# Optimization experiments

Hardware: AMD Instinct MI355X
Metric: run time of the kernel (lower is better)

Reference implementation:

```python
import jax, jax.numpy as jnp
import numpy as np
import math

B, M, N, K = 4, 8192, 8192, 16
FD = 64       # in_fdim == out_fdim (residual add)
HID = 128     # args.hidden_dim
G = 8         # args.ngroups


def index_points(points, idx):
    # points: (B, C, N), idx: (B, M, K) -> (B, C, M, K)
    return jax.vmap(lambda p, i: p[:, i])(points, idx)


def conv1d(x, w, b):  # 1x1 Conv1d: x (B,Ci,M), w (Co,Ci)
    return jnp.einsum('oi,bim->bom', w, x) + b[None, :, None]


def conv2d(x, w, b):  # 1x1 Conv2d: x (B,Ci,M,K), w (Co,Ci)
    return jnp.einsum('oi,bimk->bomk', w, x) + b[None, :, None, None]


def group_norm(x, w, b, eps=1e-5):
    # torch GroupNorm over (C//G, M, K) per group per sample
    Bb, C, Mm, Kk = x.shape
    xr = x.reshape(Bb, G, C // G, Mm, Kk)
    mu = xr.mean(axis=(2, 3, 4), keepdims=True)
    var = xr.var(axis=(2, 3, 4), keepdims=True)
    xr = (xr - mu) * jax.lax.rsqrt(var + eps)
    return xr.reshape(Bb, C, Mm, Kk) * w[None, :, None, None] + b[None, :, None, None]


def setup_inputs() -> dict:
    key = jax.random.key(0)
    ks = jax.random.split(key, 24)
    s = 0.05
    inp = {
        'q_xyzs': jax.random.normal(ks[0], (B, 3, M), jnp.float32),
        'k_xyzs': jax.random.normal(ks[1], (B, 3, N), jnp.float32),
        'q_feats': jax.random.normal(ks[2], (B, FD, M), jnp.float32),
        'k_feats': jax.random.normal(ks[3], (B, FD, N), jnp.float32),
        'v_feats': jax.random.normal(ks[4], (B, FD, N), jnp.float32),
        'knn_idx': jax.random.randint(ks[5], (B, M, K), 0, N),
        'mask': jnp.ones((B, M, K), dtype=bool),
        'wq_w': jax.random.normal(ks[6], (HID, FD)) * s, 'wq_b': jnp.zeros((HID,)),
        'wk_w': jax.random.normal(ks[7], (HID, FD)) * s, 'wk_b': jnp.zeros((HID,)),
        'wv_w': jax.random.normal(ks[8], (HID, FD)) * s, 'wv_b': jnp.zeros((HID,)),
        'd1_w': jax.random.normal(ks[9], (HID, 3)) * s, 'd1_b': jnp.zeros((HID,)),
        'dgn_w': jnp.ones((HID,)), 'dgn_b': jnp.zeros((HID,)),
        'd2_w': jax.random.normal(ks[10], (HID, HID)) * s, 'd2_b': jnp.zeros((HID,)),
        'g1_w': jax.random.normal(ks[11], (HID, HID)) * s, 'g1_b': jnp.zeros((HID,)),
        'ggn_w': jnp.ones((HID,)), 'ggn_b': jnp.zeros((HID,)),
        'g2_w': jax.random.normal(ks[12], (HID, HID)) * s, 'g2_b': jnp.zeros((HID,)),
        'post_w': jax.random.normal(ks[13], (FD, HID)) * s, 'post_b': jnp.zeros((FD,)),
    }
    return inp


def reference(q_xyzs, k_xyzs, q_feats, k_feats, v_feats, knn_idx, mask,
              wq_w, wq_b, wk_w, wk_b, wv_w, wv_b,
              d1_w, d1_b, dgn_w, dgn_b, d2_w, d2_b,
              g1_w, g1_b, ggn_w, ggn_b, g2_w, g2_b,
              post_w, post_b):
    knn_xyzs = index_points(k_xyzs, knn_idx)                 # (B,3,M,K)
    pre = q_feats
    query = conv1d(q_feats, wq_w, wq_b)                      # (B,HID,M)
    key = index_points(conv1d(k_feats, wk_w, wk_b), knn_idx) # (B,HID,M,K)
    value = index_points(conv1d(v_feats, wv_w, wv_b), knn_idx)

    rel = q_xyzs[:, :, :, None] - knn_xyzs                   # (B,3,M,K)
    pos_enc = conv2d(jax.nn.relu(group_norm(conv2d(rel, d1_w, d1_b), dgn_w, dgn_b)), d2_w, d2_b)

    attn_in = query[:, :, :, None] - key + pos_enc
    attn = conv2d(jax.nn.relu(group_norm(conv2d(attn_in, g1_w, g1_b), ggn_w, ggn_b)), g2_w, g2_b)
    attn = attn / math.sqrt(HID)
    attn = jnp.where(mask[:, None], attn, -jnp.finfo(attn.dtype).max)
    attn = jax.nn.softmax(attn, axis=-1)                     # over neighbor axis K

    res = jnp.einsum('bcmk,bcmk->bcm', attn, value + pos_enc)
    return conv1d(res, post_w, post_b) + pre
```

## Files before the change

kernel.cpp:

```cpp
#include <hip/hip_runtime.h>
#include <hip/hip_bf16.h>

typedef __attribute__((ext_vector_type(8))) short short8;
typedef __attribute__((ext_vector_type(4))) float f32x4;
typedef unsigned short ushort_t;

#define B_    4
#define M_    8192
#define N_    8192
#define KNN   16
#define FD    64
#define HID   128
#define CNT   (M_*KNN)
#define SCALE 0.08838834764831845f

#define QT_OFF       0ULL
#define KT_OFF       4194304ULL
#define VT_OFF       6291456ULL
#define WD2_OFF      8388608ULL
#define WG1_OFF      8396800ULL
#define WG2_OFF      8404992ULL
#define WQT_OFF      8413184ULL
#define WKT_OFF      8421376ULL
#define WVT_OFF      8429568ULL
#define POSTT_OFF    8437760ULL
#define G2BS_OFF     8445952ULL
#define HAFF_OFF     8446080ULL
#define RELSTATS_OFF 8448128ULL
#define YSUM_OFF     8448192ULL
#define YSQ_OFF      8448704ULL
#define GGNA_OFF     8449216ULL
#define GGNB_OFF     8449728ULL

__device__ __forceinline__ ushort_t f2bf(float x) {
    union { float f; unsigned u; } v; v.f = x;
    unsigned r = (v.u + 0x7FFFu + ((v.u >> 16) & 1u)) >> 16;
    return (ushort_t)r;
}
__device__ __forceinline__ float bf2f(ushort_t b) {
    union { unsigned u; float f; } v; v.u = ((unsigned)b) << 16;
    return v.f;
}

__global__ __launch_bounds__(256) void k_wswz(
    const float* __restrict__ d2, const float* __restrict__ g1, const float* __restrict__ g2,
    const float* __restrict__ post, const float* __restrict__ g2b,
    const float* __restrict__ wq, const float* __restrict__ wk, const float* __restrict__ wv,
    float* __restrict__ ws)
{
    int tid = blockIdx.x * 256 + threadIdx.x;
    if (tid < 16384) {
        int j = tid & 7, lane = (tid >> 3) & 63, s = (tid >> 9) & 3, ct = tid >> 11;
        int row = ct*16 + (lane & 15);
        int colk = s*32 + (lane >> 4)*8 + j;
        int si = row*HID + colk;
        ((ushort_t*)(ws + WD2_OFF))[tid] = f2bf(d2[si]);
        ((ushort_t*)(ws + WG1_OFF))[tid] = f2bf(g1[si]);
        ((ushort_t*)(ws + WG2_OFF))[tid] = f2bf(g2[si] * SCALE);
    }
    if (tid < 8192) {
        int f = tid >> 7, j = tid & 127;
        ws[POSTT_OFF + j*64 + f] = post[tid];
        int i = tid >> 7, c = tid & 127;
        ws[WQT_OFF + tid] = wq[c*FD + i];
        ws[WKT_OFF + tid] = wk[c*FD + i];
        ws[WVT_OFF + tid] = wv[c*FD + i];
    }
    if (tid < 128) ws[G2BS_OFF + tid] = g2b[tid] * SCALE;
}

__global__ __launch_bounds__(256) void k_transform(
    const float* __restrict__ qf, const float* __restrict__ kf, const float* __restrict__ vf,
    const float* __restrict__ wq_b, const float* __restrict__ wk_b, const float* __restrict__ wv_b,
    float* __restrict__ ws)
{
    __shared__ __align__(16) float sF[64*36];
    int tid = threadIdx.x;
    int t = blockIdx.y;
    int gm0 = blockIdx.x * 32;
    int b = gm0 >> 13, m0 = gm0 & (M_-1);
    const float* in = (t==0) ? qf : (t==1) ? kf : vf;
    const float* wT = ws + ((t==0) ? WQT_OFF : (t==1) ? WKT_OFF : WVT_OFF);
    const float* bi = (t==0) ? wq_b : (t==1) ? wk_b : wv_b;
    {
        int i = tid >> 2, sg = tid & 3;
        const float* src = in + ((size_t)b*FD + i)*M_ + m0 + sg*8;
        f32x4 a = *(const f32x4*)src;
        f32x4 c = *(const f32x4*)(src + 4);
        *(f32x4*)&sF[i*36 + sg*8]     = a;
        *(f32x4*)&sF[i*36 + sg*8 + 4] = c;
    }
    __syncthreads();
    int c = tid & 127, h = tid >> 7;
    float acc[16];
    float bc = bi[c];
    #pragma unroll
    for (int p = 0; p < 16; p++) acc[p] = bc;
    #pragma unroll 4
    for (int i = 0; i < 64; i++) {
        float w = wT[i*128 + c];
        #pragma unroll
        for (int pq = 0; pq < 4; pq++) {
            f32x4 fv = *(const f32x4*)&sF[i*36 + h*16 + pq*4];
            acc[pq*4+0] += w*fv[0]; acc[pq*4+1] += w*fv[1];
            acc[pq*4+2] += w*fv[2]; acc[pq*4+3] += w*fv[3];
        }
    }
    if (t == 0) {
        #pragma unroll
        for (int p = 0; p < 16; p++)
            ws[QT_OFF + (size_t)(gm0 + h*16 + p)*HID + c] = acc[p];
    } else {
        ushort_t* o = (ushort_t*)(ws + ((t==1) ? KT_OFF : VT_OFF));
        #pragma unroll
        for (int p = 0; p < 16; p++)
            o[(size_t)(gm0 + h*16 + p)*HID + c] = f2bf(acc[p]);
    }
}

__global__ __launch_bounds__(256) void k_relstats(
    const float* __restrict__ qx, const float* __restrict__ kx,
    const int* __restrict__ knn, float* __restrict__ ws)
{
    int tid = threadIdx.x;
    int b = blockIdx.y;
    int m = blockIdx.x * 256 + tid;
    const float* qb = qx + (size_t)b*3*M_;
    const float* kb = kx + (size_t)b*3*N_;
    const int* kn = knn + ((size_t)b*M_ + m)*KNN;
    float a[9] = {0,0,0,0,0,0,0,0,0};
    float q0 = qb[m], q1 = qb[M_+m], q2 = qb[2*M_+m];
    #pragma unroll
    for (int k = 0; k < KNN; k++) {
        int id = kn[k];
        float r0 = q0 - kb[id], r1 = q1 - kb[N_+id], r2 = q2 - kb[2*N_+id];
        a[0]+=r0; a[1]+=r1; a[2]+=r2;
        a[3]+=r0*r0; a[4]+=r0*r1; a[5]+=r0*r2;
        a[6]+=r1*r1; a[7]+=r1*r2; a[8]+=r2*r2;
    }
    __shared__ float red[4];
    float* rs = ws + RELSTATS_OFF + b*16;
    for (int q = 0; q < 9; q++) {
        float v = a[q];
        #pragma unroll
        for (int o = 32; o > 0; o >>= 1) v += __shfl_down(v, o, 64);
        if ((tid & 63) == 0) red[tid >> 6] = v;
        __syncthreads();
        if (tid == 0) atomicAdd(&rs[q], red[0]+red[1]+red[2]+red[3]);
        __syncthreads();
    }
}

__global__ __launch_bounds__(512) void k_dgn(
    const float* __restrict__ d1w, const float* __restrict__ d1b,
    const float* __restrict__ gw, const float* __restrict__ gb,
    float* __restrict__ ws)
{
    __shared__ float sm[512], sq[512], smu[32], srs[32];
    int t = threadIdx.x, b = t >> 7, c = t & 127;
    const float* rs = ws + RELSTATS_OFF + b*16;
    float inv = 1.0f / (float)CNT;
    float x0 = rs[0]*inv, x1 = rs[1]*inv, x2 = rs[2]*inv;
    float S00 = rs[3]*inv, S01 = rs[4]*inv, S02 = rs[5]*inv;
    float S11 = rs[6]*inv, S12 = rs[7]*inv, S22 = rs[8]*inv;
    float w0 = d1w[c*3], w1 = d1w[c*3+1], w2 = d1w[c*3+2], bc = d1b[c];
    float mc = w0*x0 + w1*x1 + w2*x2 + bc;
    float qc = w0*w0*S00 + w1*w1*S11 + w2*w2*S22
             + 2.f*(w0*w1*S01 + w0*w2*S02 + w1*w2*S12)
             + 2.f*bc*(mc - bc) + bc*bc;
    sm[t] = mc; sq[t] = qc;
    __syncthreads();
    if (t < 32) {
        int bb = t >> 3, g = t & 7;
        float mu = 0, ey = 0;
        for (int j = 0; j < 16; j++) { mu += sm[bb*128 + g*16 + j]; ey += sq[bb*128 + g*16 + j]; }
        mu *= (1.f/16.f); ey *= (1.f/16.f);
        smu[t] = mu; srs[t] = rsqrtf(ey - mu*mu + 1e-5f);
    }
    __syncthreads();
    int g = c >> 4;
    float al = gw[c] * srs[b*8 + g];
    float be = gb[c] - smu[b*8 + g] * al;
    f32x4 h; h[0] = al*w0; h[1] = al*w1; h[2] = al*w2; h[3] = al*bc + be;
    *(f32x4*)(ws + HAFF_OFF + ((size_t)b*128 + c)*4) = h;
}

__global__ __launch_bounds__(512) void k_ggn(
    const float* __restrict__ gw, const float* __restrict__ gb, float* __restrict__ ws)
{
    __shared__ float smu[32], srs[32];
    int t = threadIdx.x, b = t >> 7, c = t & 127;
    if (t < 32) {
        int bb = t >> 3, g = t & 7;
        float s1 = 0, s2 = 0;
        for (int j = 0; j < 16; j++) {
            s1 += ws[YSUM_OFF + bb*128 + g*16 + j];
            s2 += ws[YSQ_OFF  + bb*128 + g*16 + j];
        }
        float invn = 1.f / (16.f * (float)CNT);
        float mu = s1*invn, ey = s2*invn;
        smu[t] = mu; srs[t] = rsqrtf(ey - mu*mu + 1e-5f);
    }
    __syncthreads();
    int g = c >> 4;
    float al = gw[c] * srs[b*8 + g];
    float be = gb[c] - smu[b*8 + g] * al;
    ws[GGNA_OFF + b*128 + c] = al;
    ws[GGNB_OFF + b*128 + c] = be;
}

template<bool STATS>
__global__ __launch_bounds__(256, 3) void k_pipe(
    const float* __restrict__ qx, const float* __restrict__ kx, const int* __restrict__ knn,
    const float* __restrict__ qf,
    const float* __restrict__ d2b, const float* __restrict__ g1b, const float* __restrict__ postb,
    float* __restrict__ ws, float* __restrict__ out)
{
    __shared__ __align__(16) ushort_t tP[4][16*136];
    __shared__ __align__(16) ushort_t tAY[4][16*136];
    __shared__ __align__(16) f32x4 sHaff[128];
    __shared__ __align__(16) float sQR[4][128];
    __shared__ __align__(16) float sGa[128], sGb[128];
    __shared__ __align__(16) float sRel[4][16][4];
    __shared__ int sIdx[64];
    __shared__ __align__(16) float sOut[4][64];

    int tid = threadIdx.x, wid = tid >> 6, lane = tid & 63;
    int n = lane & 15, q = lane >> 4;
    int gm0 = blockIdx.x * 4;
    int b = gm0 >> 13;
    int m0 = gm0 & (M_-1);
    int ct0 = wid * 2;

    const ushort_t* ktb = (const ushort_t*)(ws + KT_OFF);
    const ushort_t* vtb = (const ushort_t*)(ws + VT_OFF);

    if (tid < 64) {
        int id = knn[(size_t)gm0*KNN + tid];
        sIdx[tid] = id;
        int p = tid >> 4, nn = tid & 15;
        int m = m0 + p;
        sRel[p][nn][0] = qx[(size_t)b*3*M_ + m]        - kx[(size_t)b*3*N_ + id];
        sRel[p][nn][1] = qx[(size_t)b*3*M_ + M_ + m]   - kx[(size_t)b*3*N_ + N_ + id];
        sRel[p][nn][2] = qx[(size_t)b*3*M_ + 2*M_ + m] - kx[(size_t)b*3*N_ + 2*N_ + id];
    }
    if (tid < 128) {
        sHaff[tid] = *(const f32x4*)(ws + HAFF_OFF + ((size_t)b*128 + tid)*4);
        if (STATS) { sGa[tid] = 0.f; sGb[tid] = 0.f; }
        else { sGa[tid] = ws[GGNA_OFF + b*128 + tid]; sGb[tid] = ws[GGNB_OFF + b*128 + tid]; }
        *(f32x4*)(&sQR[0][0] + tid*4) = *(const f32x4*)(ws + QT_OFF + (size_t)gm0*HID + tid*4);
    }
    __syncthreads();

    {
        const short8* wA = (const short8*)(ws + WD2_OFF);
        short8 wf[2][4];
        #pragma unroll
        for (int cc = 0; cc < 2; cc++)
            #pragma unroll
            for (int s = 0; s < 4; s++)
                wf[cc][s] = wA[((ct0+cc)*4 + s)*64 + lane];
        #pragma unroll
        for (int p = 0; p < 4; p++) {
            f32x4 rv = *(const f32x4*)sRel[p][n];
            short8 bh[4];
            #pragma unroll
            for (int s = 0; s < 4; s++)
                #pragma unroll
                for (int j = 0; j < 8; j++) {
                    f32x4 hf = sHaff[s*32 + q*8 + j];
                    float h = fmaf(hf[0], rv[0], fmaf(hf[1], rv[1], fmaf(hf[2], rv[2], hf[3])));
                    bh[s][j] = (short)f2bf(h > 0.f ? h : 0.f);
                }
            #pragma unroll
            for (int cc = 0; cc < 2; cc++) {
                f32x4 acc = {0.f,0.f,0.f,0.f};
                #pragma unroll
                for (int s = 0; s < 4; s++)
                    acc = __builtin_amdgcn_mfma_f32_16x16x32_bf16(wf[cc][s], bh[s], acc, 0,0,0);
                int row0 = (ct0+cc)*16 + q*4;
                f32x4 bi = *(const f32x4*)(d2b + row0);
                uint2 pv;
                pv.x = (unsigned)f2bf(acc[0]+bi[0]) | ((unsigned)f2bf(acc[1]+bi[1]) << 16);
                pv.y = (unsigned)f2bf(acc[2]+bi[2]) | ((unsigned)f2bf(acc[3]+bi[3]) << 16);
                *(uint2*)&tP[p][n*136 + row0] = pv;
            }
        }
    }
    __syncthreads();

    {
        int p = wid;
        int nn = lane >> 2, cb = lane & 3;
        int id = sIdx[p*16 + nn];
        const ushort_t* kr = ktb + ((size_t)b*N_ + id)*HID + cb*32;
        const float* qr = &sQR[p][cb*32];
        const ushort_t* pr = &tP[p][nn*136 + cb*32];
        ushort_t* ar = &tAY[p][nn*136 + cb*32];
        #pragma unroll
        for (int u = 0; u < 4; u++) {
            short8 kv = *(const short8*)(kr + u*8);
            short8 pv = *(const short8*)(pr + u*8);
            f32x4 q0 = *(const f32x4*)(qr + u*8);
            f32x4 q1 = *(const f32x4*)(qr + u*8 + 4);
            short8 av;
            #pragma unroll
            for (int j = 0; j < 8; j++) {
                float qv = (j < 4) ? q0[j] : q1[j-4];
                av[j] = (short)f2bf(qv - bf2f((ushort_t)kv[j]) + bf2f((ushort_t)pv[j]));
            }
            *(short8*)(ar + u*8) = av;
        }
    }
    __syncthreads();

    {
        const short8* wA = (const short8*)(ws + WG1_OFF);
        short8 wf[2][4];
        #pragma unroll
        for (int cc = 0; cc < 2; cc++)
            #pragma unroll
            for (int s = 0; s < 4; s++)
                wf[cc][s] = wA[((ct0+cc)*4 + s)*64 + lane];

        if (STATS) {
            float s1[2][4], s2[2][4];
            #pragma unroll
            for (int cc = 0; cc < 2; cc++)
                #pragma unroll
                for (int r = 0; r < 4; r++) { s1[cc][r] = 0.f; s2[cc][r] = 0.f; }
            f32x4 bi[2];
            bi[0] = *(const f32x4*)(g1b + (ct0+0)*16 + q*4);
            bi[1] = *(const f32x4*)(g1b + (ct0+1)*16 + q*4);
            #pragma unroll
            for (int p = 0; p < 4; p++) {
                short8 ba[4];
                #pragma unroll
                for (int s = 0; s < 4; s++)
                    ba[s] = *(const short8*)&tAY[p][n*136 + s*32 + q*8];
                #pragma unroll
                for (int cc = 0; cc < 2; cc++) {
                    f32x4 a = {0.f,0.f,0.f,0.f};
                    #pragma unroll
                    for (int s = 0; s < 4; s++)
                        a = __builtin_amdgcn_mfma_f32_16x16x32_bf16(wf[cc][s], ba[s], a, 0,0,0);
                    #pragma unroll
                    for (int r = 0; r < 4; r++) {
                        float y = a[r] + bi[cc][r];
                        s1[cc][r] += y; s2[cc][r] += y*y;
                    }
                }
            }
            #pragma unroll
            for (int cc = 0; cc < 2; cc++)
                #pragma unroll
                for (int r = 0; r < 4; r++) {
                    float v1 = s1[cc][r], v2 = s2[cc][r];
                    v1 += __shfl_xor(v1,1,64); v1 += __shfl_xor(v1,2,64);
                    v1 += __shfl_xor(v1,4,64); v1 += __shfl_xor(v1,8,64);
                    v2 += __shfl_xor(v2,1,64); v2 += __shfl_xor(v2,2,64);
                    v2 += __shfl_xor(v2,4,64); v2 += __shfl_xor(v2,8,64);
                    if (n == 0) {
                        atomicAdd(&sGa[(ct0+cc)*16 + q*4 + r], v1);
                        atomicAdd(&sGb[(ct0+cc)*16 + q*4 + r], v2);
                    }
                }
            __syncthreads();
            if (tid < 128) {
                atomicAdd(&ws[YSUM_OFF + b*128 + tid], sGa[tid]);
                atomicAdd(&ws[YSQ_OFF  + b*128 + tid], sGb[tid]);
            }
            return;
        } else {
            f32x4 acc2[4][2];
            #pragma unroll
            for (int p = 0; p < 4; p++) {
                short8 ba[4];
                #pragma unroll
                for (int s = 0; s < 4; s++)
                    ba[s] = *(const short8*)&tAY[p][n*136 + s*32 + q*8];
                #pragma unroll
                for (int cc = 0; cc < 2; cc++) {
                    f32x4 a = {0.f,0.f,0.f,0.f};
                    #pragma unroll
                    for (int s = 0; s < 4; s++)
                        a = __builtin_amdgcn_mfma_f32_16x16x32_bf16(wf[cc][s], ba[s], a, 0,0,0);
                    acc2[p][cc] = a;
                }
            }
            __syncthreads();
            #pragma unroll
            for (int p = 0; p < 4; p++)
                #pragma unroll
                for (int cc = 0; cc < 2; cc++) {
                    int row0 = (ct0+cc)*16 + q*4;
                    f32x4 bi = *(const f32x4*)(g1b + row0);
                    f32x4 ga = *(const f32x4*)&sGa[row0];
                    f32x4 gb = *(const f32x4*)&sGb[row0];
                    ushort_t yw[4];
                    #pragma unroll
                    for (int r = 0; r < 4; r++) {
                        float y = ga[r]*(acc2[p][cc][r] + bi[r]) + gb[r];
                        yw[r] = f2bf(y > 0.f ? y : 0.f);
                    }
                    uint2 yv;
                    yv.x = (unsigned)yw[0] | ((unsigned)yw[1] << 16);
                    yv.y = (unsigned)yw[2] | ((unsigned)yw[3] << 16);
                    *(uint2*)&tAY[p][n*136 + row0] = yv;
                }
            __syncthreads();
        }
    }

    {
        const short8* wA = (const short8*)(ws + WG2_OFF);
        short8 wf[2][4];
        #pragma unroll
        for (int cc = 0; cc < 2; cc++)
            #pragma unroll
            for (int s = 0; s < 4; s++)
                wf[cc][s] = wA[((ct0+cc)*4 + s)*64 + lane];
        #pragma unroll
        for (int p = 0; p < 4; p++) {
            short8 by[4];
            #pragma unroll
            for (int s = 0; s < 4; s++)
                by[s] = *(const short8*)&tAY[p][n*136 + s*32 + q*8];
            int id = sIdx[p*16 + n];
            const ushort_t* vr = vtb + ((size_t)b*N_ + id)*HID;
            #pragma unroll
            for (int cc = 0; cc < 2; cc++) {
                f32x4 a = {0.f,0.f,0.f,0.f};
                #pragma unroll
                for (int s = 0; s < 4; s++)
                    a = __builtin_amdgcn_mfma_f32_16x16x32_bf16(wf[cc][s], by[s], a, 0,0,0);
                int row0 = (ct0+cc)*16 + q*4;
                f32x4 zb = *(const f32x4*)(ws + G2BS_OFF + row0);
                uint2 vv = *(const uint2*)(vr + row0);
                uint2 pp = *(const uint2*)&tP[p][n*136 + row0];
                float e[4], num[4];
                #pragma unroll
                for (int r = 0; r < 4; r++) e[r] = __expf(a[r] + zb[r]);
                num[0] = e[0]*(bf2f((ushort_t)(vv.x & 0xffff)) + bf2f((ushort_t)(pp.x & 0xffff)));
                num[1] = e[1]*(bf2f((ushort_t)(vv.x >> 16))    + bf2f((ushort_t)(pp.x >> 16)));
                num[2] = e[2]*(bf2f((ushort_t)(vv.y & 0xffff)) + bf2f((ushort_t)(pp.y & 0xffff)));
                num[3] = e[3]*(bf2f((ushort_t)(vv.y >> 16))    + bf2f((ushort_t)(pp.y >> 16)));
                #pragma unroll
                for (int r = 0; r < 4; r++) {
                    float d = e[r], u = num[r];
                    d += __shfl_xor(d,1,64); d += __shfl_xor(d,2,64);
                    d += __shfl_xor(d,4,64); d += __shfl_xor(d,8,64);
                    u += __shfl_xor(u,1,64); u += __shfl_xor(u,2,64);
                    u += __shfl_xor(u,4,64); u += __shfl_xor(u,8,64);
                    e[r] = d; num[r] = u;
                }
                if (n == 0) {
                    f32x4 rv;
                    rv[0] = num[0]/e[0]; rv[1] = num[1]/e[1];
                    rv[2] = num[2]/e[2]; rv[3] = num[3]/e[3];
                    *(f32x4*)&sQR[p][row0] = rv;
                }
            }
        }
    }
    __syncthreads();

    {
        int p = wid, f = lane;
        const float* pt = ws + POSTT_OFF;
        const float* rr = sQR[p];
        float acc = postb[f];
        #pragma unroll 8
        for (int j = 0; j < 128; j++) acc += pt[j*64 + f] * rr[j];
        sOut[p][f] = acc;
    }
    __syncthreads();
    {
        int f = tid >> 2, msub = tid & 3;
        size_t o = (size_t)b*FD*M_ + (size_t)f*M_ + m0 + msub;
        out[o] = sOut[msub][f] + qf[o];
    }
}

extern "C" void kernel_launch(void* const* d_in, const int* in_sizes, int n_in,
                              void* d_out, int out_size, void* d_ws, size_t ws_size,
                              hipStream_t stream)
{
    const float* q_xyzs = (const float*)d_in[0];
    const float* k_xyzs = (const float*)d_in[1];
    const float* q_feats= (const float*)d_in[2];
    const float* k_feats= (const float*)d_in[3];
    const float* v_feats= (const float*)d_in[4];
    const int*   knn    = (const int*)d_in[5];
    const float* wq_w = (const float*)d_in[7];  const float* wq_b = (const float*)d_in[8];
    const float* wk_w = (const float*)d_in[9];  const float* wk_b = (const float*)d_in[10];
    const float* wv_w = (const float*)d_in[11]; const float* wv_b = (const float*)d_in[12];
    const float* d1_w = (const float*)d_in[13]; const float* d1_b = (const float*)d_in[14];
    const float* dgn_w= (const float*)d_in[15]; const float* dgn_b= (const float*)d_in[16];
    const float* d2_w = (const float*)d_in[17]; const float* d2_b = (const float*)d_in[18];
    const float* g1_w = (const float*)d_in[19]; const float* g1_b = (const float*)d_in[20];
    const float* ggn_w= (const float*)d_in[21]; const float* ggn_b= (const float*)d_in[22];
    const float* g2_w = (const float*)d_in[23]; const float* g2_b = (const float*)d_in[24];
    const float* post_w=(const float*)d_in[25]; const float* post_b=(const float*)d_in[26];
    float* ws  = (float*)d_ws;
    float* out = (float*)d_out;

    hipMemsetAsync(ws + RELSTATS_OFF, 0, 1088*sizeof(float), stream);

    k_wswz<<<64, 256, 0, stream>>>(d2_w, g1_w, g2_w, post_w, g2_b, wq_w, wk_w, wv_w, ws);
    k_transform<<<dim3(B_*M_/32, 3), 256, 0, stream>>>(
        q_feats, k_feats, v_feats, wq_b, wk_b, wv_b, ws);
    k_relstats<<<dim3(M_/256, B_), 256, 0, stream>>>(q_xyzs, k_xyzs, knn, ws);
    k_dgn<<<1, 512, 0, stream>>>(d1_w, d1_b, dgn_w, dgn_b, ws);
    k_pipe<true><<<B_*M_/4, 256, 0, stream>>>(
        q_xyzs, k_xyzs, knn, q_feats, d2_b, g1_b, post_b, ws, out);
    k_ggn<<<1, 512, 0, stream>>>(ggn_w, ggn_b, ws);
    k_pipe<false><<<B_*M_/4, 256, 0, stream>>>(
        q_xyzs, k_xyzs, knn, q_feats, d2_b, g1_b, post_b, ws, out);
}
```

Before: 574.9 us.

## Fold g1 conv into d2 and q/k projections, restructure pipe kernel

Precomputes g1·d2, g1·wq and g1·wk on device, so the g1 pre-activation is computed directly as Wfo·h + q' - k' and the separate attn_in stage and its MFMA pass go away. The stats pass now skips the d2 matmul entirely. Shared memory is unioned to allow four blocks per CU, rounding is simplified to round-half-up, and the softmax reduction is transposed so it uses fewer shuffles. The risk is bf16 rounding of the fused weight product, which changes numerics, and round-half-up bias.

```diff
diff --git a/kernel.cpp b/kernel.cpp
--- a/kernel.cpp
+++ b/kernel.cpp
@@ -18,34 +18,41 @@
 #define KT_OFF       4194304ULL
 #define VT_OFF       6291456ULL
 #define WD2_OFF      8388608ULL
-#define WG1_OFF      8396800ULL
+#define WFO_OFF      8396800ULL
 #define WG2_OFF      8404992ULL
-#define WQT_OFF      8413184ULL
-#define WKT_OFF      8421376ULL
+#define WQ2T_OFF     8413184ULL
+#define WK2T_OFF     8421376ULL
 #define WVT_OFF      8429568ULL
 #define POSTT_OFF    8437760ULL
 #define G2BS_OFF     8445952ULL
-#define HAFF_OFF     8446080ULL
-#define RELSTATS_OFF 8448128ULL
-#define YSUM_OFF     8448192ULL
-#define YSQ_OFF      8448704ULL
-#define GGNA_OFF     8449216ULL
-#define GGNB_OFF     8449728ULL
+#define BQ_OFF       8446080ULL
+#define BK_OFF       8446208ULL
+#define HAFF_OFF     8446336ULL
+#define RELSTATS_OFF 8448384ULL
+#define YSUM_OFF     8448448ULL
+#define YSQ_OFF      8448960ULL
+#define GGNA_OFF     8449472ULL
+#define GGNB_OFF     8449984ULL
 
 __device__ __forceinline__ ushort_t f2bf(float x) {
-    union { float f; unsigned u; } v; v.f = x;
-    unsigned r = (v.u + 0x7FFFu + ((v.u >> 16) & 1u)) >> 16;
-    return (ushort_t)r;
+    return (ushort_t)((__float_as_uint(x) + 0x8000u) >> 16);
+}
+__device__ __forceinline__ unsigned pk2bf(float a, float b) {
+    unsigned ua = __float_as_uint(a) + 0x8000u;
+    unsigned ub = __float_as_uint(b) + 0x8000u;
+    return (ua >> 16) | (ub & 0xFFFF0000u);
 }
 __device__ __forceinline__ float bf2f(ushort_t b) {
     union { unsigned u; float f; } v; v.u = ((unsigned)b) << 16;
     return v.f;
 }
 
-__global__ __launch_bounds__(256) void k_wswz(
+__global__ __launch_bounds__(256) void k_prep(
     const float* __restrict__ d2, const float* __restrict__ g1, const float* __restrict__ g2,
+    const float* __restrict__ wq, const float* __restrict__ wk, const float* __restrict__ wv,
     const float* __restrict__ post, const float* __restrict__ g2b,
-    const float* __restrict__ wq, const float* __restrict__ wk, const float* __restrict__ wv,
+    const float* __restrict__ wq_b, const float* __restrict__ wk_b,
+    const float* __restrict__ d2b, const float* __restrict__ g1b,
     float* __restrict__ ws)
 {
     int tid = blockIdx.x * 256 + threadIdx.x;
@@ -53,26 +60,45 @@
         int j = tid & 7, lane = (tid >> 3) & 63, s = (tid >> 9) & 3, ct = tid >> 11;
         int row = ct*16 + (lane & 15);
         int colk = s*32 + (lane >> 4)*8 + j;
-        int si = row*HID + colk;
-        ((ushort_t*)(ws + WD2_OFF))[tid] = f2bf(d2[si]);
-        ((ushort_t*)(ws + WG1_OFF))[tid] = f2bf(g1[si]);
-        ((ushort_t*)(ws + WG2_OFF))[tid] = f2bf(g2[si] * SCALE);
+        ((ushort_t*)(ws + WD2_OFF))[tid] = f2bf(d2[row*HID + colk]);
+        ((ushort_t*)(ws + WG2_OFF))[tid] = f2bf(g2[row*HID + colk] * SCALE);
+        float acc = 0.f;
+        #pragma unroll 8
+        for (int t = 0; t < HID; t++) acc += g1[row*HID + t] * d2[t*HID + colk];
+        ((ushort_t*)(ws + WFO_OFF))[tid] = f2bf(acc);
     }
     if (tid < 8192) {
         int f = tid >> 7, j = tid & 127;
         ws[POSTT_OFF + j*64 + f] = post[tid];
         int i = tid >> 7, c = tid & 127;
-        ws[WQT_OFF + tid] = wq[c*FD + i];
-        ws[WKT_OFF + tid] = wk[c*FD + i];
+        float aq = 0.f, ak = 0.f;
+        #pragma unroll 8
+        for (int h = 0; h < HID; h++) {
+            float g = g1[c*HID + h];
+            aq += g * wq[h*FD + i];
+            ak += g * wk[h*FD + i];
+        }
+        ws[WQ2T_OFF + tid] = aq;
+        ws[WK2T_OFF + tid] = ak;
         ws[WVT_OFF + tid] = wv[c*FD + i];
     }
-    if (tid < 128) ws[G2BS_OFF + tid] = g2b[tid] * SCALE;
+    if (tid < 128) {
+        ws[G2BS_OFF + tid] = g2b[tid] * SCALE;
+        float bq = g1b[tid], bk = 0.f;
+        #pragma unroll 8
+        for (int h = 0; h < HID; h++) {
+            float g = g1[tid*HID + h];
+            bq += g * (wq_b[h] + d2b[h]);
+            bk += g * wk_b[h];
+        }
+        ws[BQ_OFF + tid] = bq;
+        ws[BK_OFF + tid] = bk;
+    }
 }
 
 __global__ __launch_bounds__(256) void k_transform(
     const float* __restrict__ qf, const float* __restrict__ kf, const float* __restrict__ vf,
-    const float* __restrict__ wq_b, const float* __restrict__ wk_b, const float* __restrict__ wv_b,
-    float* __restrict__ ws)
+    const float* __restrict__ wv_b, float* __restrict__ ws)
 {
     __shared__ __align__(16) float sF[64*36];
     int tid = threadIdx.x;
@@ -80,20 +106,17 @@
     int gm0 = blockIdx.x * 32;
     int b = gm0 >> 13, m0 = gm0 & (M_-1);
     const float* in = (t==0) ? qf : (t==1) ? kf : vf;
-    const float* wT = ws + ((t==0) ? WQT_OFF : (t==1) ? WKT_OFF : WVT_OFF);
-    const float* bi = (t==0) ? wq_b : (t==1) ? wk_b : wv_b;
+    const float* wT = ws + ((t==0) ? WQ2T_OFF : (t==1) ? WK2T_OFF : WVT_OFF);
     {
         int i = tid >> 2, sg = tid & 3;
         const float* src = in + ((size_t)b*FD + i)*M_ + m0 + sg*8;
-        f32x4 a = *(const f32x4*)src;
-        f32x4 c = *(const f32x4*)(src + 4);
-        *(f32x4*)&sF[i*36 + sg*8]     = a;
-        *(f32x4*)&sF[i*36 + sg*8 + 4] = c;
+        *(f32x4*)&sF[i*36 + sg*8]     = *(const f32x4*)src;
+        *(f32x4*)&sF[i*36 + sg*8 + 4] = *(const f32x4*)(src + 4);
     }
     __syncthreads();
     int c = tid & 127, h = tid >> 7;
+    float bc = (t==0) ? ws[BQ_OFF + c] : (t==1) ? ws[BK_OFF + c] : wv_b[c];
     float acc[16];
-    float bc = bi[c];
     #pragma unroll
     for (int p = 0; p < 16; p++) acc[p] = bc;
     #pragma unroll 4
@@ -156,7 +179,7 @@
     const float* __restrict__ gw, const float* __restrict__ gb,
     float* __restrict__ ws)
 {
-    __shared__ float sm[512], sq[512], smu[32], srs[32];
+    __shared__ float sm_[512], sq_[512], smu[32], srs[32];
     int t = threadIdx.x, b = t >> 7, c = t & 127;
     const float* rs = ws + RELSTATS_OFF + b*16;
     float inv = 1.0f / (float)CNT;
@@ -168,12 +191,12 @@
     float qc = w0*w0*S00 + w1*w1*S11 + w2*w2*S22
              + 2.f*(w0*w1*S01 + w0*w2*S02 + w1*w2*S12)
              + 2.f*bc*(mc - bc) + bc*bc;
-    sm[t] = mc; sq[t] = qc;
+    sm_[t] = mc; sq_[t] = qc;
     __syncthreads();
     if (t < 32) {
         int bb = t >> 3, g = t & 7;
         float mu = 0, ey = 0;
-        for (int j = 0; j < 16; j++) { mu += sm[bb*128 + g*16 + j]; ey += sq[bb*128 + g*16 + j]; }
+        for (int j = 0; j < 16; j++) { mu += sm_[bb*128 + g*16 + j]; ey += sq_[bb*128 + g*16 + j]; }
         mu *= (1.f/16.f); ey *= (1.f/16.f);
         smu[t] = mu; srs[t] = rsqrtf(ey - mu*mu + 1e-5f);
     }
@@ -209,276 +232,234 @@
     ws[GGNB_OFF + b*128 + c] = be;
 }
 
+struct SmemPipe {
+    union {
+        ushort_t tP[4][16*136];
+        struct { f32x4 haff[128]; float rel[4][16][4]; } pre;
+    } u;
+    ushort_t tH[4][16*136];
+    float ga[128], gb[128];
+    float res[4][128];
+    int idx[64];
+};
+
 template<bool STATS>
-__global__ __launch_bounds__(256, 3) void k_pipe(
+__global__ __launch_bounds__(256, 4) void k_pipe(
     const float* __restrict__ qx, const float* __restrict__ kx, const int* __restrict__ knn,
-    const float* __restrict__ qf,
-    const float* __restrict__ d2b, const float* __restrict__ g1b, const float* __restrict__ postb,
+    const float* __restrict__ qf, const float* __restrict__ d2b, const float* __restrict__ postb,
     float* __restrict__ ws, float* __restrict__ out)
 {
-    __shared__ __align__(16) ushort_t tP[4][16*136];
-    __shared__ __align__(16) ushort_t tAY[4][16*136];
-    __shared__ __align__(16) f32x4 sHaff[128];
-    __shared__ __align__(16) float sQR[4][128];
-    __shared__ __align__(16) float sGa[128], sGb[128];
-    __shared__ __align__(16) float sRel[4][16][4];
-    __shared__ int sIdx[64];
-    __shared__ __align__(16) float sOut[4][64];
-
+    __shared__ SmemPipe sm;
     int tid = threadIdx.x, wid = tid >> 6, lane = tid & 63;
-    int n = lane & 15, q = lane >> 4;
+    int ln = lane & 15, q = lane >> 4;
     int gm0 = blockIdx.x * 4;
-    int b = gm0 >> 13;
-    int m0 = gm0 & (M_-1);
+    int b = gm0 >> 13, m0 = gm0 & (M_-1);
     int ct0 = wid * 2;
 
+    if (tid < 64) {
+        int id = knn[(size_t)gm0*KNN + tid];
+        sm.idx[tid] = id;
+        int p = tid >> 4, nn = tid & 15;
+        int m = m0 + p;
+        sm.u.pre.rel[p][nn][0] = qx[(size_t)b*3*M_ + m]        - kx[(size_t)b*3*N_ + id];
+        sm.u.pre.rel[p][nn][1] = qx[(size_t)b*3*M_ + M_ + m]   - kx[(size_t)b*3*N_ + N_ + id];
+        sm.u.pre.rel[p][nn][2] = qx[(size_t)b*3*M_ + 2*M_ + m] - kx[(size_t)b*3*N_ + 2*N_ + id];
+    }
+    if (tid < 128) {
+        sm.u.pre.haff[tid] = *(const f32x4*)(ws + HAFF_OFF + ((size_t)b*128 + tid)*4);
+        if (STATS) { sm.ga[tid] = 0.f; sm.gb[tid] = 0.f; }
+        else { sm.ga[tid] = ws[GGNA_OFF + b*128 + tid]; sm.gb[tid] = ws[GGNB_OFF + b*128 + tid]; }
+    }
+    __syncthreads();
+
+    {
+        int p = tid >> 6, n = (tid >> 2) & 15, cb = tid & 3;
+        float r0 = sm.u.pre.rel[p][n][0];
+        float r1 = sm.u.pre.rel[p][n][1];
+        float r2 = sm.u.pre.rel[p][n][2];
+        unsigned* dst = (unsigned*)&sm.tH[p][n*136 + cb*32];
+        #pragma unroll
+        for (int jj = 0; jj < 32; jj += 2) {
+            f32x4 h1 = sm.u.pre.haff[cb*32 + jj];
+            f32x4 h2 = sm.u.pre.haff[cb*32 + jj + 1];
+            float a = fmaf(h1[0], r0, fmaf(h1[1], r1, fmaf(h1[2], r2, h1[3])));
+            float c = fmaf(h2[0], r0, fmaf(h2[1], r1, fmaf(h2[2], r2, h2[3])));
+            dst[jj >> 1] = pk2bf(a > 0.f ? a : 0.f, c > 0.f ? c : 0.f);
+        }
+    }
+    __syncthreads();
+
+    const short8* wd2 = (const short8*)(ws + WD2_OFF);
+    const short8* wfo = (const short8*)(ws + WFO_OFF);
     const ushort_t* ktb = (const ushort_t*)(ws + KT_OFF);
     const ushort_t* vtb = (const ushort_t*)(ws + VT_OFF);
 
-    if (tid < 64) {
-        int id = knn[(size_t)gm0*KNN + tid];
-        sIdx[tid] = id;
-        int p = tid >> 4, nn = tid & 15;
-        int m = m0 + p;
-        sRel[p][nn][0] = qx[(size_t)b*3*M_ + m]        - kx[(size_t)b*3*N_ + id];
-        sRel[p][nn][1] = qx[(size_t)b*3*M_ + M_ + m]   - kx[(size_t)b*3*N_ + N_ + id];
-        sRel[p][nn][2] = qx[(size_t)b*3*M_ + 2*M_ + m] - kx[(size_t)b*3*N_ + 2*N_ + id];
-    }
-    if (tid < 128) {
-        sHaff[tid] = *(const f32x4*)(ws + HAFF_OFF + ((size_t)b*128 + tid)*4);
-        if (STATS) { sGa[tid] = 0.f; sGb[tid] = 0.f; }
-        else { sGa[tid] = ws[GGNA_OFF + b*128 + tid]; sGb[tid] = ws[GGNB_OFF + b*128 + tid]; }
-        *(f32x4*)(&sQR[0][0] + tid*4) = *(const f32x4*)(ws + QT_OFF + (size_t)gm0*HID + tid*4);
-    }
-    __syncthreads();
-
-    {
-        const short8* wA = (const short8*)(ws + WD2_OFF);
-        short8 wf[2][4];
+    f32x4 bid2[2], gav[2], gbv[2];
+    if (!STATS) {
+        #pragma unroll
+        for (int cc = 0; cc < 2; cc++) {
+            int row0 = (ct0+cc)*16 + q*4;
+            bid2[cc] = *(const f32x4*)(d2b + row0);
+            gav[cc] = *(const f32x4*)&sm.ga[row0];
+            gbv[cc] = *(const f32x4*)&sm.gb[row0];
+        }
+    }
+    float s1[2][4], s2[2][4];
+    if (STATS) {
         #pragma unroll
         for (int cc = 0; cc < 2; cc++)
             #pragma unroll
+            for (int r = 0; r < 4; r++) { s1[cc][r] = 0.f; s2[cc][r] = 0.f; }
+    }
+
+    for (int p = 0; p < 4; p++) {
+        int gm = gm0 + p;
+        short8 bh[4];
+        #pragma unroll
+        for (int s = 0; s < 4; s++)
+            bh[s] = *(const short8*)&sm.tH[p][ln*136 + s*32 + q*8];
+
+        f32x4 accY[2];
+        #pragma unroll
+        for (int cc = 0; cc < 2; cc++) {
+            f32x4 a = {0.f,0.f,0.f,0.f};
+            #pragma unroll
             for (int s = 0; s < 4; s++)
-                wf[cc][s] = wA[((ct0+cc)*4 + s)*64 + lane];
-        #pragma unroll
-        for (int p = 0; p < 4; p++) {
-            f32x4 rv = *(const f32x4*)sRel[p][n];
-            short8 bh[4];
-            #pragma unroll
-            for (int s = 0; s < 4; s++)
-                #pragma unroll
-                for (int j = 0; j < 8; j++) {
-                    f32x4 hf = sHaff[s*32 + q*8 + j];
-                    float h = fmaf(hf[0], rv[0], fmaf(hf[1], rv[1], fmaf(hf[2], rv[2], hf[3])));
-                    bh[s][j] = (short)f2bf(h > 0.f ? h : 0.f);
-                }
-            #pragma unroll
-            for (int cc = 0; cc < 2; cc++) {
-                f32x4 acc = {0.f,0.f,0.f,0.f};
-                #pragma unroll
-                for (int s = 0; s < 4; s++)
-                    acc = __builtin_amdgcn_mfma_f32_16x16x32_bf16(wf[cc][s], bh[s], acc, 0,0,0);
-                int row0 = (ct0+cc)*16 + q*4;
-                f32x4 bi = *(const f32x4*)(d2b + row0);
-                uint2 pv;
-                pv.x = (unsigned)f2bf(acc[0]+bi[0]) | ((unsigned)f2bf(acc[1]+bi[1]) << 16);
-                pv.y = (unsigned)f2bf(acc[2]+bi[2]) | ((unsigned)f2bf(acc[3]+bi[3]) << 16);
-                *(uint2*)&tP[p][n*136 + row0] = pv;
-            }
-        }
-    }
-    __syncthreads();
-
-    {
-        int p = wid;
-        int nn = lane >> 2, cb = lane & 3;
-        int id = sIdx[p*16 + nn];
-        const ushort_t* kr = ktb + ((size_t)b*N_ + id)*HID + cb*32;
-        const float* qr = &sQR[p][cb*32];
-        const ushort_t* pr = &tP[p][nn*136 + cb*32];
-        ushort_t* ar = &tAY[p][nn*136 + cb*32];
-        #pragma unroll
-        for (int u = 0; u < 4; u++) {
-            short8 kv = *(const short8*)(kr + u*8);
-            short8 pv = *(const short8*)(pr + u*8);
-            f32x4 q0 = *(const f32x4*)(qr + u*8);
-            f32x4 q1 = *(const f32x4*)(qr + u*8 + 4);
-            short8 av;
-            #pragma unroll
-            for (int j = 0; j < 8; j++) {
-                float qv = (j < 4) ? q0[j] : q1[j-4];
-                av[j] = (short)f2bf(qv - bf2f((ushort_t)kv[j]) + bf2f((ushort_t)pv[j]));
-            }
-            *(short8*)(ar + u*8) = av;
-        }
-    }
-    __syncthreads();
-
-    {
-        const short8* wA = (const short8*)(ws + WG1_OFF);
-        short8 wf[2][4];
-        #pragma unroll
-        for (int cc = 0; cc < 2; cc++)
-            #pragma unroll
-            for (int s = 0; s < 4; s++)
-                wf[cc][s] = wA[((ct0+cc)*4 + s)*64 + lane];
-
-        if (STATS) {
-            float s1[2][4], s2[2][4];
-            #pragma unroll
-            for (int cc = 0; cc < 2; cc++)
-                #pragma unroll
-                for (int r = 0; r < 4; r++) { s1[cc][r] = 0.f; s2[cc][r] = 0.f; }
-            f32x4 bi[2];
-            bi[0] = *(const f32x4*)(g1b + (ct0+0)*16 + q*4);
-            bi[1] = *(const f32x4*)(g1b + (ct0+1)*16 + q*4);
-            #pragma unroll
-            for (int p = 0; p < 4; p++) {
-                short8 ba[4];
-                #pragma unroll
-                for (int s = 0; s < 4; s++)
-                    ba[s] = *(const short8*)&tAY[p][n*136 + s*32 + q*8];
-                #pragma unroll
-                for (int cc = 0; cc < 2; cc++) {
-                    f32x4 a = {0.f,0.f,0.f,0.f};
-                    #pragma unroll
-                    for (int s = 0; s < 4; s++)
-                        a = __builtin_amdgcn_mfma_f32_16x16x32_bf16(wf[cc][s], ba[s], a, 0,0,0);
-                    #pragma unroll
-                    for (int r = 0; r < 4; r++) {
-                        float y = a[r] + bi[cc][r];
-                        s1[cc][r] += y; s2[cc][r] += y*y;
-                    }
-                }
-            }
-            #pragma unroll
-            for (int cc = 0; cc < 2; cc++)
-                #pragma unroll
-                for (int r = 0; r < 4; r++) {
-                    float v1 = s1[cc][r], v2 = s2[cc][r];
-                    v1 += __shfl_xor(v1,1,64); v1 += __shfl_xor(v1,2,64);
-                    v1 += __shfl_xor(v1,4,64); v1 += __shfl_xor(v1,8,64);
-                    v2 += __shfl_xor(v2,1,64); v2 += __shfl_xor(v2,2,64);
-                    v2 += __shfl_xor(v2,4,64); v2 += __shfl_xor(v2,8,64);
-                    if (n == 0) {
-                        atomicAdd(&sGa[(ct0+cc)*16 + q*4 + r], v1);
-                        atomicAdd(&sGb[(ct0+cc)*16 + q*4 + r], v2);
-                    }
-                }
-            __syncthreads();
-            if (tid < 128) {
-                atomicAdd(&ws[YSUM_OFF + b*128 + tid], sGa[tid]);
-                atomicAdd(&ws[YSQ_OFF  + b*128 + tid], sGb[tid]);
-            }
-            return;
-        } else {
-            f32x4 acc2[4][2];
-            #pragma unroll
-            for (int p = 0; p < 4; p++) {
-                short8 ba[4];
-                #pragma unroll
-                for (int s = 0; s < 4; s++)
-                    ba[s] = *(const short8*)&tAY[p][n*136 + s*32 + q*8];
-                #pragma unroll
-                for (int cc = 0; cc < 2; cc++) {
-                    f32x4 a = {0.f,0.f,0.f,0.f};
-                    #pragma unroll
-                    for (int s = 0; s < 4; s++)
-                        a = __builtin_amdgcn_mfma_f32_16x16x32_bf16(wf[cc][s], ba[s], a, 0,0,0);
-                    acc2[p][cc] = a;
-                }
-            }
-            __syncthreads();
-            #pragma unroll
-            for (int p = 0; p < 4; p++)
-                #pragma unroll
-                for (int cc = 0; cc < 2; cc++) {
-                    int row0 = (ct0+cc)*16 + q*4;
-                    f32x4 bi = *(const f32x4*)(g1b + row0);
-                    f32x4 ga = *(const f32x4*)&sGa[row0];
-                    f32x4 gb = *(const f32x4*)&sGb[row0];
-                    ushort_t yw[4];
-                    #pragma unroll
-                    for (int r = 0; r < 4; r++) {
-                        float y = ga[r]*(acc2[p][cc][r] + bi[r]) + gb[r];
-                        yw[r] = f2bf(y > 0.f ? y : 0.f);
-                    }
-                    uint2 yv;
-                    yv.x = (unsigned)yw[0] | ((unsigned)yw[1] << 16);
-                    yv.y = (unsigned)yw[2] | ((unsigned)yw[3] << 16);
-                    *(uint2*)&tAY[p][n*136 + row0] = yv;
-                }
-            __syncthreads();
-        }
-    }
-
-    {
-        const short8* wA = (const short8*)(ws + WG2_OFF);
-        short8 wf[2][4];
-        #pragma unroll
-        for (int cc = 0; cc < 2; cc++)
-            #pragma unroll
-            for (int s = 0; s < 4; s++)
-                wf[cc][s] = wA[((ct0+cc)*4 + s)*64 + lane];
-        #pragma unroll
-        for (int p = 0; p < 4; p++) {
-            short8 by[4];
-            #pragma unroll
-            for (int s = 0; s < 4; s++)
-                by[s] = *(const short8*)&tAY[p][n*136 + s*32 + q*8];
-            int id = sIdx[p*16 + n];
-            const ushort_t* vr = vtb + ((size_t)b*N_ + id)*HID;
+                a = __builtin_amdgcn_mfma_f32_16x16x32_bf16(wfo[((ct0+cc)*4+s)*64 + lane], bh[s], a, 0,0,0);
+            accY[cc] = a;
+        }
+        if (!STATS) {
             #pragma unroll
             for (int cc = 0; cc < 2; cc++) {
                 f32x4 a = {0.f,0.f,0.f,0.f};
                 #pragma unroll
                 for (int s = 0; s < 4; s++)
-                    a = __builtin_amdgcn_mfma_f32_16x16x32_bf16(wf[cc][s], by[s], a, 0,0,0);
+                    a = __builtin_amdgcn_mfma_f32_16x16x32_bf16(wd2[((ct0+cc)*4+s)*64 + lane], bh[s], a, 0,0,0);
                 int row0 = (ct0+cc)*16 + q*4;
-                f32x4 zb = *(const f32x4*)(ws + G2BS_OFF + row0);
-                uint2 vv = *(const uint2*)(vr + row0);
-                uint2 pp = *(const uint2*)&tP[p][n*136 + row0];
-                float e[4], num[4];
+                uint2 pv;
+                pv.x = pk2bf(a[0]+bid2[cc][0], a[1]+bid2[cc][1]);
+                pv.y = pk2bf(a[2]+bid2[cc][2], a[3]+bid2[cc][3]);
+                *(uint2*)&sm.u.tP[p][ln*136 + row0] = pv;
+            }
+        }
+        int id = sm.idx[p*16 + ln];
+        float yv[2][4];
+        #pragma unroll
+        for (int cc = 0; cc < 2; cc++) {
+            int row0 = (ct0+cc)*16 + q*4;
+            f32x4 qv = *(const f32x4*)(ws + QT_OFF + (size_t)gm*HID + row0);
+            uint2 kv = *(const uint2*)(ktb + ((size_t)b*N_ + id)*HID + row0);
+            yv[cc][0] = accY[cc][0] + qv[0] - bf2f((ushort_t)(kv.x & 0xffff));
+            yv[cc][1] = accY[cc][1] + qv[1] - bf2f((ushort_t)(kv.x >> 16));
+            yv[cc][2] = accY[cc][2] + qv[2] - bf2f((ushort_t)(kv.y & 0xffff));
+            yv[cc][3] = accY[cc][3] + qv[3] - bf2f((ushort_t)(kv.y >> 16));
+        }
+        if (STATS) {
+            #pragma unroll
+            for (int cc = 0; cc < 2; cc++)
                 #pragma unroll
-                for (int r = 0; r < 4; r++) e[r] = __expf(a[r] + zb[r]);
-                num[0] = e[0]*(bf2f((ushort_t)(vv.x & 0xffff)) + bf2f((ushort_t)(pp.x & 0xffff)));
-                num[1] = e[1]*(bf2f((ushort_t)(vv.x >> 16))    + bf2f((ushort_t)(pp.x >> 16)));
-                num[2] = e[2]*(bf2f((ushort_t)(vv.y & 0xffff)) + bf2f((ushort_t)(pp.y & 0xffff)));
-                num[3] = e[3]*(bf2f((ushort_t)(vv.y >> 16))    + bf2f((ushort_t)(pp.y >> 16)));
+                for (int r = 0; r < 4; r++) { s1[cc][r] += yv[cc][r]; s2[cc][r] += yv[cc][r]*yv[cc][r]; }
+        } else {
+            __syncthreads();
+            #pragma unroll
+            for (int cc = 0; cc < 2; cc++) {
+                int row0 = (ct0+cc)*16 + q*4;
+                float y0 = fmaf(gav[cc][0], yv[cc][0], gbv[cc][0]);
+                float y1 = fmaf(gav[cc][1], yv[cc][1], gbv[cc][1]);
+                float y2 = fmaf(gav[cc][2], yv[cc][2], gbv[cc][2]);
+                float y3 = fmaf(gav[cc][3], yv[cc][3], gbv[cc][3]);
+                uint2 yw;
+                yw.x = pk2bf(y0 > 0.f ? y0 : 0.f, y1 > 0.f ? y1 : 0.f);
+                yw.y = pk2bf(y2 > 0.f ? y2 : 0.f, y3 > 0.f ? y3 : 0.f);
+                *(uint2*)&sm.tH[p][ln*136 + row0] = yw;
+            }
+        }
+    }
+
+    if (STATS) {
+        #pragma unroll
+        for (int cc = 0; cc < 2; cc++)
+            #pragma unroll
+            for (int r = 0; r < 4; r++) {
+                float v1 = s1[cc][r], v2 = s2[cc][r];
+                v1 += __shfl_xor(v1,1,64); v1 += __shfl_xor(v1,2,64);
+                v1 += __shfl_xor(v1,4,64); v1 += __shfl_xor(v1,8,64);
+                v2 += __shfl_xor(v2,1,64); v2 += __shfl_xor(v2,2,64);
+                v2 += __shfl_xor(v2,4,64); v2 += __shfl_xor(v2,8,64);
+                if (ln == 0) {
+                    atomicAdd(&sm.ga[(ct0+cc)*16 + q*4 + r], v1);
+                    atomicAdd(&sm.gb[(ct0+cc)*16 + q*4 + r], v2);
+                }
+            }
+        __syncthreads();
+        if (tid < 128) {
+            atomicAdd(&ws[YSUM_OFF + b*128 + tid], sm.ga[tid]);
+            atomicAdd(&ws[YSQ_OFF  + b*128 + tid], sm.gb[tid]);
+        }
+        return;
+    }
+
+    {
+        int p = tid >> 6, n = (tid >> 2) & 15, cb = tid & 3;
+        int id = sm.idx[p*16 + n];
+        const ushort_t* vr = vtb + ((size_t)b*N_ + id)*HID + cb*32;
+        ushort_t* pr = &sm.u.tP[p][n*136 + cb*32];
+        #pragma unroll
+        for (int u = 0; u < 4; u++) {
+            short8 vv = *(const short8*)(vr + u*8);
+            short8 pp = *(const short8*)(pr + u*8);
+            unsigned w[4];
+            #pragma unroll
+            for (int j = 0; j < 4; j++) {
+                float a = bf2f((ushort_t)vv[j*2])   + bf2f((ushort_t)pp[j*2]);
+                float c = bf2f((ushort_t)vv[j*2+1]) + bf2f((ushort_t)pp[j*2+1]);
+                w[j] = pk2bf(a, c);
+            }
+            *(short8*)(pr + u*8) = *(short8*)w;
+        }
+    }
+    __syncthreads();
+
+    {
+        const short8* wg2 = (const short8*)(ws + WG2_OFF);
+        #pragma unroll
+        for (int p = 0; p < 4; p++) {
+            short8 ay[4];
+            #pragma unroll
+            for (int s = 0; s < 4; s++)
+                ay[s] = *(const short8*)&sm.tH[p][ln*136 + s*32 + q*8];
+            #pragma unroll
+            for (int cc = 0; cc < 2; cc++) {
+                int cout = (ct0+cc)*16 + ln;
+                f32x4 a = {0.f,0.f,0.f,0.f};
+                #pragma unroll
+                for (int s = 0; s < 4; s++)
+                    a = __builtin_amdgcn_mfma_f32_16x16x32_bf16(ay[s], wg2[((ct0+cc)*4+s)*64 + lane], a, 0,0,0);
+                float zb = ws[G2BS_OFF + cout];
+                float den = 0.f, num = 0.f;
                 #pragma unroll
                 for (int r = 0; r < 4; r++) {
-                    float d = e[r], u = num[r];
-                    d += __shfl_xor(d,1,64); d += __shfl_xor(d,2,64);
-                    d += __shfl_xor(d,4,64); d += __shfl_xor(d,8,64);
-                    u += __shfl_xor(u,1,64); u += __shfl_xor(u,2,64);
-                    u += __shfl_xor(u,4,64); u += __shfl_xor(u,8,64);
-                    e[r] = d; num[r] = u;
+                    float e = __expf(a[r] + zb);
+                    den += e;
+                    num += e * bf2f(sm.u.tP[p][(q*4+r)*136 + cout]);
                 }
-                if (n == 0) {
-                    f32x4 rv;
-                    rv[0] = num[0]/e[0]; rv[1] = num[1]/e[1];
-                    rv[2] = num[2]/e[2]; rv[3] = num[3]/e[3];
-                    *(f32x4*)&sQR[p][row0] = rv;
-                }
+                den += __shfl_xor(den, 16, 64); den += __shfl_xor(den, 32, 64);
+                num += __shfl_xor(num, 16, 64); num += __shfl_xor(num, 32, 64);
+                if (q == 0) sm.res[p][cout] = num / den;
             }
         }
     }
     __syncthreads();
 
     {
-        int p = wid, f = lane;
+        int f = tid >> 2, p = tid & 3;
         const float* pt = ws + POSTT_OFF;
-        const float* rr = sQR[p];
+        const float* rr = sm.res[p];
         float acc = postb[f];
         #pragma unroll 8
         for (int j = 0; j < 128; j++) acc += pt[j*64 + f] * rr[j];
-        sOut[p][f] = acc;
-    }
-    __syncthreads();
-    {
-        int f = tid >> 2, msub = tid & 3;
-        size_t o = (size_t)b*FD*M_ + (size_t)f*M_ + m0 + msub;
-        out[o] = sOut[msub][f] + qf[o];
+        size_t o = (size_t)b*FD*M_ + (size_t)f*M_ + m0 + p;
+        out[o] = acc + qf[o];
     }
 }
 
@@ -507,14 +488,14 @@
 
     hipMemsetAsync(ws + RELSTATS_OFF, 0, 1088*sizeof(float), stream);
 
-    k_wswz<<<64, 256, 0, stream>>>(d2_w, g1_w, g2_w, post_w, g2_b, wq_w, wk_w, wv_w, ws);
-    k_transform<<<dim3(B_*M_/32, 3), 256, 0, stream>>>(
-        q_feats, k_feats, v_feats, wq_b, wk_b, wv_b, ws);
+    k_prep<<<64, 256, 0, stream>>>(d2_w, g1_w, g2_w, wq_w, wk_w, wv_w,
+                                   post_w, g2_b, wq_b, wk_b, d2_b, g1_b, ws);
+    k_transform<<<dim3(B_*M_/32, 3), 256, 0, stream>>>(q_feats, k_feats, v_feats, wv_b, ws);
     k_relstats<<<dim3(M_/256, B_), 256, 0, stream>>>(q_xyzs, k_xyzs, knn, ws);
     k_dgn<<<1, 512, 0, stream>>>(d1_w, d1_b, dgn_w, dgn_b, ws);
     k_pipe<true><<<B_*M_/4, 256, 0, stream>>>(
-        q_xyzs, k_xyzs, knn, q_feats, d2_b, g1_b, post_b, ws, out);
+        q_xyzs, k_xyzs, knn, q_feats, d2_b, post_b, ws, out);
     k_ggn<<<1, 512, 0, stream>>>(ggn_w, ggn_b, ws);
     k_pipe<false><<<B_*M_/4, 256, 0, stream>>>(
-        q_xyzs, k_xyzs, knn, q_feats, d2_b, g1_b, post_b, ws, out);
-}
+        q_xyzs, k_xyzs, knn, q_feats, d2_b, post_b, ws, out);
+}
```

Result: faster. 527.0 us (-8.3%).
